# Optimization experiments

Hardware: AMD Instinct MI355X
Metric: run time of the kernel (lower is better)

The kernel has to match this reference:

```python
import jax, jax.numpy as jnp
import numpy as np
from jax import lax

L, D, H, F, T = 4, 512, 8, 2048, 1000
B, S = 8, 1024

def setup_inputs() -> dict:
    key = jax.random.key(0)
    ks = jax.random.split(key, 12)
    s = 0.02
    return {
        'features': jax.random.normal(ks[0], (B, S, D), jnp.float32),
        'Wq': jax.random.normal(ks[1], (L, D, D), jnp.float32) * s,
        'Wk': jax.random.normal(ks[2], (L, D, D), jnp.float32) * s,
        'Wv': jax.random.normal(ks[3], (L, D, D), jnp.float32) * s,
        'bq': jnp.zeros((L, D), jnp.float32),
        'bk': jnp.zeros((L, D), jnp.float32),
        'bv': jnp.zeros((L, D), jnp.float32),
        'Wo': jax.random.normal(ks[4], (L, D, D), jnp.float32) * s,
        'bo': jnp.zeros((L, D), jnp.float32),
        'ln1_g': jnp.ones((L, D), jnp.float32),
        'ln1_b': jnp.zeros((L, D), jnp.float32),
        'ln2_g': jnp.ones((L, D), jnp.float32),
        'ln2_b': jnp.zeros((L, D), jnp.float32),
        'W1': jax.random.normal(ks[5], (L, F, D), jnp.float32) * s,
        'b1': jnp.zeros((L, F), jnp.float32),
        'W2': jax.random.normal(ks[6], (L, D, F), jnp.float32) * s,
        'b2': jnp.zeros((L, D), jnp.float32),
        'Wout': jax.random.normal(ks[7], (D, D), jnp.float32) * s,
        'bout': jnp.zeros((D,), jnp.float32),
    }

def _layernorm(x, g, b, eps=1e-5):
    mu = jnp.mean(x, axis=-1, keepdims=True)
    var = jnp.var(x, axis=-1, keepdims=True)
    return (x - mu) / jnp.sqrt(var + eps) * g + b

def _ddim_noise(features):
    betas = jnp.linspace(1e-4, 0.02, T)
    alphas_cumprod = jnp.cumprod(1.0 - betas)
    base = jax.random.key(42)
    def step(x, t):
        a = alphas_cumprod[t]
        noise = jax.random.normal(jax.random.fold_in(base, t), x.shape, x.dtype)
        return jnp.sqrt(a) * x + jnp.sqrt(1.0 - a) * noise, None
    x, _ = lax.scan(step, features, jnp.arange(1, T))
    return x

def reference(features, Wq, Wk, Wv, bq, bk, bv, Wo, bo, ln1_g, ln1_b, ln2_g, ln2_b, W1, b1, W2, b2, Wout, bout):
    x = _ddim_noise(features)  # [B,S,D]
    dh = D // H
    scale = 1.0 / jnp.sqrt(jnp.float32(dh))
    for l in range(L):
        # multi-head self-attention (post-norm, no dropout at eval)
        q = (x @ Wq[l].T + bq[l]).reshape(B, S, H, dh).transpose(0, 2, 1, 3)
        k = (x @ Wk[l].T + bk[l]).reshape(B, S, H, dh).transpose(0, 2, 1, 3)
        v = (x @ Wv[l].T + bv[l]).reshape(B, S, H, dh).transpose(0, 2, 1, 3)
        scores = jnp.einsum('bhqd,bhkd->bhqk', q, k) * scale
        attn = jax.nn.softmax(scores, axis=-1)
        o = jnp.einsum('bhqk,bhkd->bhqd', attn, v).transpose(0, 2, 1, 3).reshape(B, S, D)
        o = o @ Wo[l].T + bo[l]
        x = _layernorm(x + o, ln1_g[l], ln1_b[l])
        # feed-forward (ReLU, PyTorch default)
        ff = jax.nn.relu(x @ W1[l].T + b1[l]) @ W2[l].T + b2[l]
        x = _layernorm(x + ff, ln2_g[l], ln2_b[l])
    return x @ Wout.T + bout
```

## Files before the change

### kernel.cpp

```cpp
#include <hip/hip_runtime.h>
#include <stdint.h>
#include <math.h>

typedef unsigned short u16;
typedef __bf16 bf16x8 __attribute__((ext_vector_type(8)));
typedef float f32x4 __attribute__((ext_vector_type(4)));
typedef short s16x8 __attribute__((ext_vector_type(8)));
union B8 { s16x8 s; bf16x8 b; };

__device__ __forceinline__ u16 f2bf(float f) {
    union { __bf16 h; u16 u; } r;
    r.h = (__bf16)f;
    return r.u;
}
__device__ __forceinline__ uint32_t pk2bf(float a, float b) {
    union { __bf16 h[2]; uint32_t u; } r;
    r.h[0] = (__bf16)a; r.h[1] = (__bf16)b;
    return r.u;
}
__device__ __forceinline__ float fexp2(float x) {
    return __builtin_amdgcn_exp2f(x);
}

typedef const __attribute__((address_space(1))) uint32_t* gas_t;
typedef __attribute__((address_space(3))) uint32_t* las_t;
__device__ __forceinline__ void gld16(const void* g, void* l) {
    __builtin_amdgcn_global_load_lds((gas_t)g, (las_t)l, 16, 0, 0);
}

__host__ __forceinline__ uint32_t rotl32(uint32_t x, int d) {
    return (x << d) | (x >> (32 - d));
}
__device__ __forceinline__ uint32_t rotl_d(uint32_t x, int d) {
    return __builtin_amdgcn_alignbit(x, x, (uint32_t)(32 - d));
}

__host__ inline void tf2x32_h(uint32_t k0, uint32_t k1, uint32_t& x0, uint32_t& x1) {
    uint32_t k2 = k0 ^ k1 ^ 0x1BD11BDAu;
    x0 += k0; x1 += k1;
    x0 += x1; x1 = rotl32(x1, 13); x1 ^= x0;
    x0 += x1; x1 = rotl32(x1, 15); x1 ^= x0;
    x0 += x1; x1 = rotl32(x1, 26); x1 ^= x0;
    x0 += x1; x1 = rotl32(x1,  6); x1 ^= x0;
    x0 += k1; x1 += k2 + 1u;
    x0 += x1; x1 = rotl32(x1, 17); x1 ^= x0;
    x0 += x1; x1 = rotl32(x1, 29); x1 ^= x0;
    x0 += x1; x1 = rotl32(x1, 16); x1 ^= x0;
    x0 += x1; x1 = rotl32(x1, 24); x1 ^= x0;
    x0 += k2; x1 += k0 + 2u;
    x0 += x1; x1 = rotl32(x1, 13); x1 ^= x0;
    x0 += x1; x1 = rotl32(x1, 15); x1 ^= x0;
    x0 += x1; x1 = rotl32(x1, 26); x1 ^= x0;
    x0 += x1; x1 = rotl32(x1,  6); x1 ^= x0;
    x0 += k0; x1 += k1 + 3u;
    x0 += x1; x1 = rotl32(x1, 17); x1 ^= x0;
    x0 += x1; x1 = rotl32(x1, 29); x1 ^= x0;
    x0 += x1; x1 = rotl32(x1, 16); x1 ^= x0;
    x0 += x1; x1 = rotl32(x1, 24); x1 ^= x0;
    x0 += k1; x1 += k2 + 4u;
    x0 += x1; x1 = rotl32(x1, 13); x1 ^= x0;
    x0 += x1; x1 = rotl32(x1, 15); x1 ^= x0;
    x0 += x1; x1 = rotl32(x1, 26); x1 ^= x0;
    x0 += x1; x1 = rotl32(x1,  6); x1 ^= x0;
    x0 += k2; x1 += k0 + 5u;
}

__device__ __forceinline__ void tf2x32_d(uint32_t k0, uint32_t k1,
                                         uint32_t& x0, uint32_t& x1) {
    uint32_t k2 = k0 ^ k1 ^ 0x1BD11BDAu;
    x0 += k0; x1 += k1;
    x0 += x1; x1 = rotl_d(x1, 13); x1 ^= x0;
    x0 += x1; x1 = rotl_d(x1, 15); x1 ^= x0;
    x0 += x1; x1 = rotl_d(x1, 26); x1 ^= x0;
    x0 += x1; x1 = rotl_d(x1,  6); x1 ^= x0;
    x0 += k1; x1 += k2 + 1u;
    x0 += x1; x1 = rotl_d(x1, 17); x1 ^= x0;
    x0 += x1; x1 = rotl_d(x1, 29); x1 ^= x0;
    x0 += x1; x1 = rotl_d(x1, 16); x1 ^= x0;
    x0 += x1; x1 = rotl_d(x1, 24); x1 ^= x0;
    x0 += k2; x1 += k0 + 2u;
    x0 += x1; x1 = rotl_d(x1, 13); x1 ^= x0;
    x0 += x1; x1 = rotl_d(x1, 15); x1 ^= x0;
    x0 += x1; x1 = rotl_d(x1, 26); x1 ^= x0;
    x0 += x1; x1 = rotl_d(x1,  6); x1 ^= x0;
    x0 += k0; x1 += k1 + 3u;
    x0 += x1; x1 = rotl_d(x1, 17); x1 ^= x0;
    x0 += x1; x1 = rotl_d(x1, 29); x1 ^= x0;
    x0 += x1; x1 = rotl_d(x1, 16); x1 ^= x0;
    x0 += x1; x1 = rotl_d(x1, 24); x1 ^= x0;
    x0 += k1; x1 += k2 + 4u;
    x0 += x1; x1 = rotl_d(x1, 13); x1 ^= x0;
    x0 += x1; x1 = rotl_d(x1, 15); x1 ^= x0;
    x0 += x1; x1 = rotl_d(x1, 26); x1 ^= x0;
    x0 += x1; x1 = rotl_d(x1,  6); x1 ^= x0;
    x0 += k2; x1 += k0 + 5u;
}

__device__ __forceinline__ float erfinv_f(float x) {
    float w = -__logf(fmaf(x, -x, 1.0f));
    float p;
    if (w < 5.0f) {
        w = w - 2.5f;
        p = 2.81022636e-08f;
        p = p * w + 3.43273939e-07f;
        p = p * w + -3.5233877e-06f;
        p = p * w + -4.39150654e-06f;
        p = p * w + 0.00021858087f;
        p = p * w + -0.00125372503f;
        p = p * w + -0.00417768164f;
        p = p * w + 0.246640727f;
        p = p * w + 1.50140941f;
    } else {
        w = sqrtf(w) - 3.0f;
        p = -0.000200214257f;
        p = p * w + 0.000100950558f;
        p = p * w + 0.00134934322f;
        p = p * w + -0.00367342844f;
        p = p * w + 0.00573950773f;
        p = p * w + -0.0076224613f;
        p = p * w + 0.00943887047f;
        p = p * w + 1.00167406f;
        p = p * w + 2.83297682f;
    }
    return p * x;
}

__device__ __forceinline__ float tf_normal(uint32_t k0, uint32_t k1, uint32_t idx) {
    uint32_t x0 = 0u, x1 = idx;
    tf2x32_d(k0, k1, x0, x1);
    uint32_t bits = x0 ^ x1;
    float f = __uint_as_float((bits >> 9) | 0x3f800000u) - 1.0f;
    float u = f * 2.0f - 0.99999994f;
    u = fmaxf(-0.99999994f, u);
    return 1.41421354f * erfinv_f(u);
}

__global__ __launch_bounds__(256) void noise_kernel(
    float* __restrict__ x, u16* __restrict__ xb,
    uint32_t ka0, uint32_t ka1, float ca,
    uint32_t kb0, uint32_t kb1, float cb, int n4)
{
    int i = blockIdx.x * 256 + threadIdx.x;
    if (i >= n4) return;
    float4 vx;
    ushort4 vb;
    #pragma unroll
    for (int e = 0; e < 4; ++e) {
        uint32_t idx = (uint32_t)(i * 4 + e);
        float a = ca * tf_normal(ka0, ka1, idx)
                + cb * tf_normal(kb0, kb1, idx);
        (&vx.x)[e] = a;
        (&vb.x)[e] = f2bf(a);
    }
    ((float4*)x)[i] = vx;
    ((ushort4*)xb)[i] = vb;
}

__global__ __launch_bounds__(256) void cvt_bf16_kernel(
    const float* __restrict__ s, u16* __restrict__ d, int n4)
{
    int i = blockIdx.x * 256 + threadIdx.x;
    if (i >= n4) return;
    float4 v = ((const float4*)s)[i];
    uint2 o;
    o.x = pk2bf(v.x, v.y);
    o.y = pk2bf(v.z, v.w);
    ((uint2*)d)[i] = o;
}

__global__ __launch_bounds__(256) void cvt_qkvw_kernel(
    const float* __restrict__ Wq, const float* __restrict__ Wk,
    const float* __restrict__ Wv, u16* __restrict__ dst, int n4)
{
    int i = blockIdx.x * 256 + threadIdx.x;
    if (i >= n4) return;
    int e = i * 4;
    int l = e / 786432;
    int rem = e - l * 786432;
    int sel = rem >> 18;
    int off = rem & 262143;
    const float* src = (sel == 0 ? Wq : sel == 1 ? Wk : Wv) + l * 262144 + off;
    float4 v = *(const float4*)src;
    uint2 o;
    o.x = pk2bf(v.x, v.y);
    o.y = pk2bf(v.z, v.w);
    *(uint2*)(dst + e) = o;
}

template<int TN, bool DBUF, bool QKV, bool RELU, bool RESID, bool BF16OUT>
__global__ __launch_bounds__(256) void gemm_bt(
    const u16* __restrict__ A, const u16* __restrict__ Bw,
    const float* __restrict__ bias0, const float* __restrict__ bias1,
    const float* __restrict__ bias2, const float* __restrict__ resid,
    void* __restrict__ out0, void* __restrict__ out1, void* __restrict__ out2,
    int M, int N, int K)
{
    constexpr int ACH = 16;
    constexpr int BCH = TN / 8;
    constexpr int CPW = (ACH + BCH) / 4;
    constexpr int NF = TN / 32;
    constexpr int NBUF = DBUF ? 2 : 1;
    constexpr int ASZ = 128 * 64;
    constexpr int BSZ = TN * 64;
    __shared__ __align__(16) u16 At[NBUF * ASZ];
    __shared__ __align__(16) u16 Bt[NBUF * BSZ];
    const int tid = threadIdx.x;
    const int l = tid & 63;
    const int w = tid >> 6;
    const int wr = w >> 1, wc = w & 1;

    int lid = blockIdx.y * gridDim.x + blockIdx.x;
    int nwg = gridDim.x * gridDim.y;
    int mb, nb;
    if ((nwg & 7) == 0) {
        int nlid = (lid & 7) * (nwg >> 3) + (lid >> 3);
        mb = nlid / gridDim.x;
        nb = nlid - mb * gridDim.x;
    } else { mb = blockIdx.y; nb = blockIdx.x; }

    const int lrow = l >> 3;
    const int lch  = (l & 7) ^ lrow;

    const u16* aTile = A  + (size_t)(mb * 128) * K + (size_t)lrow * K + lch * 8;
    const u16* bTile = Bw + (size_t)(nb * TN) * K + (size_t)lrow * K + lch * 8;

    f32x4 acc[4][NF] = {};

    auto stage = [&](int buf, int k0) {
        #pragma unroll
        for (int i = 0; i < CPW; ++i) {
            int c = w * CPW + i;
            if (c < ACH) gld16(aTile + (size_t)(c * 8) * K + k0, &At[buf * ASZ + c * 512]);
            else gld16(bTile + (size_t)((c - ACH) * 8) * K + k0, &Bt[buf * BSZ + (c - ACH) * 512]);
        }
    };
    auto compute = [&](int buf) {
        const u16* Ac = &At[buf * ASZ];
        const u16* Bc = &Bt[buf * BSZ];
        #pragma unroll
        for (int kc = 0; kc < 2; ++kc) {
            B8 af[4], bfr[NF];
            #pragma unroll
            for (int m = 0; m < 4; ++m) {
                int r = wr * 64 + m * 16 + (l & 15);
                int ch = kc * 4 + (l >> 4);
                af[m].s = *(const s16x8*)&Ac[r * 64 + ((ch ^ (r & 7)) * 8)];
            }
            #pragma unroll
            for (int n = 0; n < NF; ++n) {
                int r = wc * (TN / 2) + n * 16 + (l & 15);
                int ch = kc * 4 + (l >> 4);
                bfr[n].s = *(const s16x8*)&Bc[r * 64 + ((ch ^ (r & 7)) * 8)];
            }
            #pragma unroll
            for (int m = 0; m < 4; ++m)
                #pragma unroll
                for (int n = 0; n < NF; ++n)
                    acc[m][n] = __builtin_amdgcn_mfma_f32_16x16x32_bf16(
                        af[m].b, bfr[n].b, acc[m][n], 0, 0, 0);
        }
    };

    if constexpr (DBUF) {
        stage(0, 0);
        __syncthreads();
        int cur = 0;
        for (int k0 = 0; k0 < K; k0 += 64) {
            if (k0 + 64 < K) stage(cur ^ 1, k0 + 64);
            compute(cur);
            __syncthreads();
            cur ^= 1;
        }
    } else {
        for (int k0 = 0; k0 < K; k0 += 64) {
            stage(0, k0);
            __syncthreads();
            compute(0);
            __syncthreads();
        }
    }

    const float* biasp;
    void* outp;
    int colbase, Nout;
    float oscale = 1.0f;
    if constexpr (QKV) {
        int which = nb >> 2;
        colbase = (nb & 3) * 128 + wc * 64;
        if (which == 2) {
            float bcol[NF];
            #pragma unroll
            for (int n = 0; n < NF; ++n)
                bcol[n] = bias2[colbase + n * 16 + (l & 15)];
            u16* vT = (u16*)out2;
            #pragma unroll
            for (int m = 0; m < 4; ++m) {
                int row0 = mb * 128 + wr * 64 + m * 16 + (l >> 4) * 4;
                int bb = row0 >> 10, s0 = row0 & 1023;
                #pragma unroll
                for (int n = 0; n < NF; ++n) {
                    int col = colbase + n * 16 + (l & 15);
                    int hh = col >> 6, dd = col & 63;
                    uint2 o;
                    o.x = pk2bf(acc[m][n][0] + bcol[n], acc[m][n][1] + bcol[n]);
                    o.y = pk2bf(acc[m][n][2] + bcol[n], acc[m][n][3] + bcol[n]);
                    *(uint2*)&vT[((size_t)((bb * 8 + hh) * 64 + dd)) * 1024 + s0] = o;
                }
            }
            return;
        }
        biasp = which == 0 ? bias0 : bias1;
        outp  = which == 0 ? out0  : out1;
        if (which == 0) oscale = 0.18033688f;
        Nout = 512;
    } else {
        colbase = nb * TN + wc * (TN / 2);
        biasp = bias0;
        outp = out0;
        Nout = N;
    }

    float bcol[NF];
    #pragma unroll
    for (int n = 0; n < NF; ++n)
        bcol[n] = biasp[colbase + n * 16 + (l & 15)];

    #pragma unroll
    for (int m = 0; m < 4; ++m) {
        #pragma unroll
        for (int j = 0; j < 4; ++j) {
            int row = mb * 128 + wr * 64 + m * 16 + (l >> 4) * 4 + j;
            #pragma unroll
            for (int n = 0; n < NF; ++n) {
                int col = colbase + n * 16 + (l & 15);
                float v = acc[m][n][j] + bcol[n];
                if constexpr (QKV) v *= oscale;
                if constexpr (RESID) v += resid[(size_t)row * Nout + col];
                if constexpr (RELU)  v = fmaxf(v, 0.0f);
                if constexpr (BF16OUT) ((u16*)outp)[(size_t)row * Nout + col] = f2bf(v);
                else                   ((float*)outp)[(size_t)row * Nout + col] = v;
            }
        }
    }
}

template<bool RESID>
__global__ __launch_bounds__(512) void gemm64(
    const u16* __restrict__ A, const u16* __restrict__ Bw,
    const float* __restrict__ bias, const float* __restrict__ resid,
    float* __restrict__ out, int N, int K)
{
    constexpr int ACH = 16;
    constexpr int ASZ = 128 * 64, BSZ = 64 * 64;
    __shared__ __align__(16) u16 At[2 * ASZ];
    __shared__ __align__(16) u16 Bt[2 * BSZ];
    const int tid = threadIdx.x;
    const int l = tid & 63;
    const int w = tid >> 6;
    const int wr = w >> 1, wc = w & 1;

    int lid = blockIdx.y * gridDim.x + blockIdx.x;
    int nwg = gridDim.x * gridDim.y;
    int nlid = (lid & 7) * (nwg >> 3) + (lid >> 3);
    int mb = nlid / gridDim.x;
    int nb = nlid - mb * gridDim.x;

    const int lrow = l >> 3;
    const int lch  = (l & 7) ^ lrow;

    const u16* aTile = A  + (size_t)(mb * 128) * K + (size_t)lrow * K + lch * 8;
    const u16* bTile = Bw + (size_t)(nb * 64) * K + (size_t)lrow * K + lch * 8;

    f32x4 acc[2][2] = {};

    auto stage = [&](int buf, int k0) {
        #pragma unroll
        for (int i = 0; i < 3; ++i) {
            int c = w * 3 + i;
            if (c < ACH) gld16(aTile + (size_t)(c * 8) * K + k0, &At[buf * ASZ + c * 512]);
            else gld16(bTile + (size_t)((c - ACH) * 8) * K + k0, &Bt[buf * BSZ + (c - ACH) * 512]);
        }
    };
    auto compute = [&](int buf) {
        const u16* Ac = &At[buf * ASZ];
        const u16* Bc = &Bt[buf * BSZ];
        #pragma unroll
        for (int kc = 0; kc < 2; ++kc) {
            B8 af[2], bfr[2];
            #pragma unroll
            for (int m = 0; m < 2; ++m) {
                int r = wr * 32 + m * 16 + (l & 15);
                int ch = kc * 4 + (l >> 4);
                af[m].s = *(const s16x8*)&Ac[r * 64 + ((ch ^ (r & 7)) * 8)];
            }
            #pragma unroll
            for (int n = 0; n < 2; ++n) {
                int r = wc * 32 + n * 16 + (l & 15);
                int ch = kc * 4 + (l >> 4);
                bfr[n].s = *(const s16x8*)&Bc[r * 64 + ((ch ^ (r & 7)) * 8)];
            }
            #pragma unroll
            for (int m = 0; m < 2; ++m)
                #pragma unroll
                for (int n = 0; n < 2; ++n)
                    acc[m][n] = __builtin_amdgcn_mfma_f32_16x16x32_bf16(
                        af[m].b, bfr[n].b, acc[m][n], 0, 0, 0);
        }
    };

    stage(0, 0);
    __syncthreads();
    int cur = 0;
    for (int k0 = 0; k0 < K; k0 += 64) {
        if (k0 + 64 < K) stage(cur ^ 1, k0 + 64);
        compute(cur);
        __syncthreads();
        cur ^= 1;
    }

    float bcol[2];
    #pragma unroll
    for (int n = 0; n < 2; ++n)
        bcol[n] = bias[nb * 64 + wc * 32 + n * 16 + (l & 15)];

    #pragma unroll
    for (int m = 0; m < 2; ++m) {
        #pragma unroll
        for (int j = 0; j < 4; ++j) {
            int row = mb * 128 + wr * 32 + m * 16 + (l >> 4) * 4 + j;
            #pragma unroll
            for (int n = 0; n < 2; ++n) {
                int col = nb * 64 + wc * 32 + n * 16 + (l & 15);
                float v = acc[m][n][j] + bcol[n];
                if constexpr (RESID) v += resid[(size_t)row * N + col];
                out[(size_t)row * N + col] = v;
            }
        }
    }
}

__global__ __launch_bounds__(256) void ln_kernel(
    float* __restrict__ x, const float* __restrict__ g, const float* __restrict__ b,
    u16* __restrict__ xb)
{
    int row = blockIdx.x * 4 + (threadIdx.x >> 6);
    int l = threadIdx.x & 63;
    float4* xr = (float4*)(x + row * 512);
    float4 v0 = xr[l];
    float4 v1 = xr[l + 64];
    float s = v0.x + v0.y + v0.z + v0.w + v1.x + v1.y + v1.z + v1.w;
    float q = v0.x * v0.x + v0.y * v0.y + v0.z * v0.z + v0.w * v0.w
            + v1.x * v1.x + v1.y * v1.y + v1.z * v1.z + v1.w * v1.w;
    #pragma unroll
    for (int m = 1; m < 64; m <<= 1) {
        s += __shfl_xor(s, m, 64);
        q += __shfl_xor(q, m, 64);
    }
    float mean = s * (1.0f / 512.0f);
    float var  = q * (1.0f / 512.0f) - mean * mean;
    float rstd = rsqrtf(var + 1e-5f);
    const float4* gv = (const float4*)g;
    const float4* bv = (const float4*)b;
    float4 g0 = gv[l], g1 = gv[l + 64], b0 = bv[l], b1 = bv[l + 64];
    float4 o0, o1;
    o0.x = (v0.x - mean) * rstd * g0.x + b0.x;
    o0.y = (v0.y - mean) * rstd * g0.y + b0.y;
    o0.z = (v0.z - mean) * rstd * g0.z + b0.z;
    o0.w = (v0.w - mean) * rstd * g0.w + b0.w;
    o1.x = (v1.x - mean) * rstd * g1.x + b1.x;
    o1.y = (v1.y - mean) * rstd * g1.y + b1.y;
    o1.z = (v1.z - mean) * rstd * g1.z + b1.z;
    o1.w = (v1.w - mean) * rstd * g1.w + b1.w;
    xr[l] = o0; xr[l + 64] = o1;
    uint2 h0, h1;
    h0.x = pk2bf(o0.x, o0.y); h0.y = pk2bf(o0.z, o0.w);
    h1.x = pk2bf(o1.x, o1.y); h1.y = pk2bf(o1.z, o1.w);
    ((uint2*)(xb + row * 512))[l] = h0;
    ((uint2*)(xb + row * 512))[l + 64] = h1;
}

__global__ __launch_bounds__(512) void attn_kernel(
    const u16* __restrict__ Q, const u16* __restrict__ Km,
    const u16* __restrict__ vT, u16* __restrict__ O)
{
    __shared__ __align__(16) u16 Kt[2][64 * 64];
    __shared__ __align__(16) u16 Vt[2][64 * 64];
    __shared__ __align__(16) char Pl[8][4096];
    const int tid = threadIdx.x;
    const int l = tid & 63;
    const int w = tid >> 6;
    const int g = l >> 4;
    const int q15 = l & 15;
    const int bh = blockIdx.x;
    const int qb = blockIdx.y;
    const int b = bh >> 3, h = bh & 7;
    const int rowQ0 = b * 1024 + qb * 256 + w * 32;
    const int colh = h * 64;
    char* pl = &Pl[w][0];

    const int srow = l >> 3;
    const u16* Kbase = Km + (size_t)(b * 1024) * 512 + colh;
    const u16* Vbase = vT + (size_t)bh * 64 * 1024;

    B8 qf[2][2];
    #pragma unroll
    for (int qt = 0; qt < 2; ++qt)
        #pragma unroll
        for (int kc = 0; kc < 2; ++kc)
            qf[qt][kc].s = *(const s16x8*)&Q[(size_t)(rowQ0 + qt * 16 + q15) * 512
                                            + colh + kc * 32 + g * 8];

    f32x4 oacc[4][2] = {};
    float lrun[2] = {0.0f, 0.0f};

    auto stage = [&](int buf, int kt) {
        int r = w * 8 + srow;
        int cc = (l & 7) ^ (r & 7);
        gld16(Kbase + (size_t)(kt * 64 + r) * 512 + cc * 8, &Kt[buf][w * 512]);
        gld16(Vbase + (size_t)r * 1024 + kt * 64 + cc * 8, &Vt[buf][w * 512]);
    };

    stage(0, 0);
    __syncthreads();
    int cur = 0;

    for (int kt = 0; kt < 16; ++kt) {
        if (kt < 15) stage(cur ^ 1, kt + 1);
        const u16* KtL = &Kt[cur][0];
        const u16* VtL = &Vt[cur][0];

        f32x4 st[2][4];
        #pragma unroll
        for (int mt = 0; mt < 4; ++mt) {
            int r = mt * 16 + q15;
            B8 kf0, kf1;
            kf0.s = *(const s16x8*)&KtL[r * 64 + ((g ^ (r & 7)) * 8)];
            kf1.s = *(const s16x8*)&KtL[r * 64 + (((4 + g) ^ (r & 7)) * 8)];
            #pragma unroll
            for (int qt = 0; qt < 2; ++qt) {
                f32x4 t = {0.f, 0.f, 0.f, 0.f};
                t = __builtin_amdgcn_mfma_f32_16x16x32_bf16(kf0.b, qf[qt][0].b, t, 0, 0, 0);
                t = __builtin_amdgcn_mfma_f32_16x16x32_bf16(kf1.b, qf[qt][1].b, t, 0, 0, 0);
                st[qt][mt] = t;
            }
        }

        #pragma unroll
        for (int qt = 0; qt < 2; ++qt) {
            int qrow = qt * 16 + q15;
            int rbase = qrow * 128;
            int sw = (qrow & 7) << 4;
            float rs = 0.0f;
            #pragma unroll
            for (int mt = 0; mt < 4; ++mt) {
                float e0 = fexp2(st[qt][mt][0]);
                float e1 = fexp2(st[qt][mt][1]);
                float e2 = fexp2(st[qt][mt][2]);
                float e3 = fexp2(st[qt][mt][3]);
                rs += (e0 + e1) + (e2 + e3);
                uint2 pk;
                pk.x = pk2bf(e0, e1);
                pk.y = pk2bf(e2, e3);
                *(uint2*)(pl + rbase + ((mt * 32 + g * 8) ^ sw)) = pk;
            }
            rs += __shfl_xor(rs, 16, 64);
            rs += __shfl_xor(rs, 32, 64);
            lrun[qt] += rs;
        }

        B8 pf[2][2];
        #pragma unroll
        for (int qt = 0; qt < 2; ++qt) {
            int qrow = qt * 16 + q15;
            int sw = (qrow & 7) << 4;
            pf[qt][0].s = *(const s16x8*)(pl + qrow * 128 + ((g * 16) ^ sw));
            pf[qt][1].s = *(const s16x8*)(pl + qrow * 128 + (((4 + g) * 16) ^ sw));
        }

        #pragma unroll
        for (int dt = 0; dt < 4; ++dt) {
            int r = dt * 16 + q15;
            B8 vf0, vf1;
            vf0.s = *(const s16x8*)&VtL[r * 64 + ((g ^ (r & 7)) * 8)];
            vf1.s = *(const s16x8*)&VtL[r * 64 + (((4 + g) ^ (r & 7)) * 8)];
            #pragma unroll
            for (int qt = 0; qt < 2; ++qt) {
                oacc[dt][qt] = __builtin_amdgcn_mfma_f32_16x16x32_bf16(
                    vf0.b, pf[qt][0].b, oacc[dt][qt], 0, 0, 0);
                oacc[dt][qt] = __builtin_amdgcn_mfma_f32_16x16x32_bf16(
                    vf1.b, pf[qt][1].b, oacc[dt][qt], 0, 0, 0);
            }
        }
        __syncthreads();
        cur ^= 1;
    }

    #pragma unroll
    for (int qt = 0; qt < 2; ++qt) {
        float inv = 1.0f / lrun[qt];
        int row = rowQ0 + qt * 16 + q15;
        #pragma unroll
        for (int dt = 0; dt < 4; ++dt) {
            uint2 o;
            o.x = pk2bf(oacc[dt][qt][0] * inv, oacc[dt][qt][1] * inv);
            o.y = pk2bf(oacc[dt][qt][2] * inv, oacc[dt][qt][3] * inv);
            *(uint2*)&O[(size_t)row * 512 + colh + dt * 16 + g * 4] = o;
        }
    }
}

extern "C" void kernel_launch(void* const* d_in, const int* in_sizes, int n_in,
                              void* d_out, int out_size, void* d_ws, size_t ws_size,
                              hipStream_t stream)
{
    const int D = 512, F = 2048, Lc = 4;
    const int Mrows = 8 * 1024;

    const float* Wq   = (const float*)d_in[1];
    const float* Wk   = (const float*)d_in[2];
    const float* Wv   = (const float*)d_in[3];
    const float* bq   = (const float*)d_in[4];
    const float* bk   = (const float*)d_in[5];
    const float* bv   = (const float*)d_in[6];
    const float* Wo   = (const float*)d_in[7];
    const float* bo   = (const float*)d_in[8];
    const float* ln1g = (const float*)d_in[9];
    const float* ln1b = (const float*)d_in[10];
    const float* ln2g = (const float*)d_in[11];
    const float* ln2b = (const float*)d_in[12];
    const float* W1   = (const float*)d_in[13];
    const float* b1   = (const float*)d_in[14];
    const float* W2   = (const float*)d_in[15];
    const float* b2   = (const float*)d_in[16];
    const float* Wout = (const float*)d_in[17];
    const float* bout = (const float*)d_in[18];

    char* p = (char*)d_ws;
    auto alloc = [&](size_t bytes) {
        char* r = p;
        p += (bytes + 255) & ~(size_t)255;
        return r;
    };
    float* xA = (float*)alloc((size_t)Mrows * D * 4);
    float* xB = (float*)alloc((size_t)Mrows * D * 4);
    u16* xb   = (u16*)alloc((size_t)Mrows * D * 2);
    char* pool = alloc((size_t)Mrows * F * 2);
    u16* qb_ = (u16*)pool;
    u16* kb_ = (u16*)(pool + (size_t)Mrows * D * 2);
    u16* vT  = (u16*)(pool + (size_t)Mrows * D * 2 * 2);
    u16* ao  = (u16*)(pool + (size_t)Mrows * D * 2 * 3);
    u16* ff1 = (u16*)pool;
    u16* wqkvB = (u16*)alloc((size_t)Lc * 3 * D * D * 2);
    u16* woB   = (u16*)alloc((size_t)Lc * D * D * 2);
    u16* w1B   = (u16*)alloc((size_t)Lc * F * D * 2);
    u16* w2B   = (u16*)alloc((size_t)Lc * D * F * 2);
    u16* woutB = (u16*)alloc((size_t)D * D * 2);

    auto cvt = [&](const float* src, u16* dst, size_t n) {
        int n4 = (int)(n / 4);
        cvt_bf16_kernel<<<(n4 + 255) / 256, 256, 0, stream>>>(src, dst, n4);
    };
    {
        int n4 = Lc * 3 * D * D / 4;
        cvt_qkvw_kernel<<<(n4 + 255) / 256, 256, 0, stream>>>(Wq, Wk, Wv, wqkvB, n4);
    }
    cvt(Wo, woB, (size_t)Lc * D * D);
    cvt(W1, w1B, (size_t)Lc * F * D);
    cvt(W2, w2B, (size_t)Lc * D * F);
    cvt(Wout, woutB, (size_t)D * D);

    float ac[1000];
    {
        float start = 1e-4f, stop = 0.02f;
        float delta = (stop - start) / 999.0f;
        float prod = 1.0f;
        for (int i = 0; i < 1000; ++i) {
            float beta = start + (float)i * delta;
            prod *= (1.0f - beta);
            ac[i] = prod;
        }
    }
    int ts[2] = {999, 998};
    double cs[2];
    double tail = 1.0;
    for (int idx = 0; idx < 2; ++idx) {
        int t = ts[idx];
        cs[idx] = sqrt(1.0 - (double)ac[t]) * tail;
        tail *= sqrt((double)ac[t]);
    }
    uint32_t kk[2][2];
    for (int idx = 0; idx < 2; ++idx) {
        uint32_t x0 = 0u, x1 = (uint32_t)ts[idx];
        tf2x32_h(0u, 42u, x0, x1);
        kk[idx][0] = x0; kk[idx][1] = x1;
    }
    int n4tot = Mrows * D / 4;
    noise_kernel<<<(n4tot + 255) / 256, 256, 0, stream>>>(
        xA, xb,
        kk[0][0], kk[0][1], (float)cs[0],
        kk[1][0], kk[1][1], (float)cs[1], n4tot);

    dim3 gqkv(3 * D / 128, Mrows / 128);
    dim3 g64(D / 64, Mrows / 128);
    dim3 gff1(F / 128, Mrows / 128);

    for (int l = 0; l < Lc; ++l) {
        const u16* wqkv_l = wqkvB + (size_t)l * 3 * D * D;
        const u16* wo_l = woB + (size_t)l * D * D;
        const u16* w1_l = w1B + (size_t)l * F * D;
        const u16* w2_l = w2B + (size_t)l * D * F;

        gemm_bt<128, false, true, false, false, true><<<gqkv, 256, 0, stream>>>(
            xb, wqkv_l, bq + l * D, bk + l * D, bv + l * D, nullptr,
            qb_, kb_, vT, Mrows, 3 * D, D);
        attn_kernel<<<dim3(64, 4), 512, 0, stream>>>(qb_, kb_, vT, ao);
        gemm64<true><<<g64, 512, 0, stream>>>(
            ao, wo_l, bo + l * D, xA, xB, D, D);
        ln_kernel<<<Mrows / 4, 256, 0, stream>>>(xB, ln1g + l * D, ln1b + l * D, xb);
        gemm_bt<128, false, false, true, false, true><<<gff1, 256, 0, stream>>>(
            xb, w1_l, b1 + l * F, nullptr, nullptr, nullptr,
            ff1, nullptr, nullptr, Mrows, F, D);
        gemm64<true><<<g64, 512, 0, stream>>>(
            ff1, w2_l, b2 + l * D, xB, xA, D, F);
        ln_kernel<<<Mrows / 4, 256, 0, stream>>>(xA, ln2g + l * D, ln2b + l * D, xb);
    }
    gemm64<false><<<g64, 512, 0, stream>>>(
        xb, woutB, bout, nullptr, (float*)d_out, D, D);
}
```

Baseline: 616.1 us.

## Keep residual stream in bf16 and fuse weight conversions into one kernel

Drops the fp32 copies of the hidden state and uses the existing bf16 buffer as the residual input. The output projections now write bf16 pre-norm sums, and layernorm reads bf16 and writes only bf16. The five weight-conversion launches become a single kernel over one contiguous buffer. This cuts global memory traffic and launch count, but keeping the residual in bf16 loses precision across layers. Unused double-buffer template paths are also removed.

```diff
diff --git a/kernel.cpp b/kernel.cpp
--- a/kernel.cpp
+++ b/kernel.cpp
@@ -17,6 +17,9 @@
     union { __bf16 h[2]; uint32_t u; } r;
     r.h[0] = (__bf16)a; r.h[1] = (__bf16)b;
     return r.u;
+}
+__device__ __forceinline__ float bf2f(u16 u) {
+    return __uint_as_float(((uint32_t)u) << 16);
 }
 __device__ __forceinline__ float fexp2(float x) {
     return __builtin_amdgcn_exp2f(x);
@@ -136,50 +139,43 @@
 }
 
 __global__ __launch_bounds__(256) void noise_kernel(
-    float* __restrict__ x, u16* __restrict__ xb,
+    u16* __restrict__ xb,
     uint32_t ka0, uint32_t ka1, float ca,
     uint32_t kb0, uint32_t kb1, float cb, int n4)
 {
     int i = blockIdx.x * 256 + threadIdx.x;
     if (i >= n4) return;
-    float4 vx;
     ushort4 vb;
     #pragma unroll
     for (int e = 0; e < 4; ++e) {
         uint32_t idx = (uint32_t)(i * 4 + e);
         float a = ca * tf_normal(ka0, ka1, idx)
                 + cb * tf_normal(kb0, kb1, idx);
-        (&vx.x)[e] = a;
         (&vb.x)[e] = f2bf(a);
     }
-    ((float4*)x)[i] = vx;
     ((ushort4*)xb)[i] = vb;
 }
 
-__global__ __launch_bounds__(256) void cvt_bf16_kernel(
-    const float* __restrict__ s, u16* __restrict__ d, int n4)
-{
-    int i = blockIdx.x * 256 + threadIdx.x;
-    if (i >= n4) return;
-    float4 v = ((const float4*)s)[i];
-    uint2 o;
-    o.x = pk2bf(v.x, v.y);
-    o.y = pk2bf(v.z, v.w);
-    ((uint2*)d)[i] = o;
-}
-
-__global__ __launch_bounds__(256) void cvt_qkvw_kernel(
+__global__ __launch_bounds__(256) void cvt_all_kernel(
     const float* __restrict__ Wq, const float* __restrict__ Wk,
-    const float* __restrict__ Wv, u16* __restrict__ dst, int n4)
+    const float* __restrict__ Wv, const float* __restrict__ Wo,
+    const float* __restrict__ W1, const float* __restrict__ W2,
+    const float* __restrict__ Wout, u16* __restrict__ dst, int n4)
 {
     int i = blockIdx.x * 256 + threadIdx.x;
     if (i >= n4) return;
     int e = i * 4;
-    int l = e / 786432;
-    int rem = e - l * 786432;
-    int sel = rem >> 18;
-    int off = rem & 262143;
-    const float* src = (sel == 0 ? Wq : sel == 1 ? Wk : Wv) + l * 262144 + off;
+    const float* src;
+    if (e < 3145728) {
+        int l = e / 786432;
+        int rem = e - l * 786432;
+        int sel = rem >> 18;
+        int off = rem & 262143;
+        src = (sel == 0 ? Wq : sel == 1 ? Wk : Wv) + l * 262144 + off;
+    } else if (e < 4194304) src = Wo + (e - 3145728);
+    else if (e < 8388608)  src = W1 + (e - 4194304);
+    else if (e < 12582912) src = W2 + (e - 8388608);
+    else                   src = Wout + (e - 12582912);
     float4 v = *(const float4*)src;
     uint2 o;
     o.x = pk2bf(v.x, v.y);
@@ -187,11 +183,11 @@
     *(uint2*)(dst + e) = o;
 }
 
-template<int TN, bool DBUF, bool QKV, bool RELU, bool RESID, bool BF16OUT>
+template<int TN, bool QKV, bool RELU>
 __global__ __launch_bounds__(256) void gemm_bt(
     const u16* __restrict__ A, const u16* __restrict__ Bw,
     const float* __restrict__ bias0, const float* __restrict__ bias1,
-    const float* __restrict__ bias2, const float* __restrict__ resid,
+    const float* __restrict__ bias2,
     void* __restrict__ out0, void* __restrict__ out1, void* __restrict__ out2,
     int M, int N, int K)
 {
@@ -199,11 +195,10 @@
     constexpr int BCH = TN / 8;
     constexpr int CPW = (ACH + BCH) / 4;
     constexpr int NF = TN / 32;
-    constexpr int NBUF = DBUF ? 2 : 1;
     constexpr int ASZ = 128 * 64;
     constexpr int BSZ = TN * 64;
-    __shared__ __align__(16) u16 At[NBUF * ASZ];
-    __shared__ __align__(16) u16 Bt[NBUF * BSZ];
+    __shared__ __align__(16) u16 At[ASZ];
+    __shared__ __align__(16) u16 Bt[BSZ];
     const int tid = threadIdx.x;
     const int l = tid & 63;
     const int w = tid >> 6;
@@ -226,17 +221,14 @@
 
     f32x4 acc[4][NF] = {};
 
-    auto stage = [&](int buf, int k0) {
+    for (int k0 = 0; k0 < K; k0 += 64) {
         #pragma unroll
         for (int i = 0; i < CPW; ++i) {
             int c = w * CPW + i;
-            if (c < ACH) gld16(aTile + (size_t)(c * 8) * K + k0, &At[buf * ASZ + c * 512]);
-            else gld16(bTile + (size_t)((c - ACH) * 8) * K + k0, &Bt[buf * BSZ + (c - ACH) * 512]);
-        }
-    };
-    auto compute = [&](int buf) {
-        const u16* Ac = &At[buf * ASZ];
-        const u16* Bc = &Bt[buf * BSZ];
+            if (c < ACH) gld16(aTile + (size_t)(c * 8) * K + k0, &At[c * 512]);
+            else gld16(bTile + (size_t)((c - ACH) * 8) * K + k0, &Bt[(c - ACH) * 512]);
+        }
+        __syncthreads();
         #pragma unroll
         for (int kc = 0; kc < 2; ++kc) {
             B8 af[4], bfr[NF];
@@ -244,13 +236,13 @@
             for (int m = 0; m < 4; ++m) {
                 int r = wr * 64 + m * 16 + (l & 15);
                 int ch = kc * 4 + (l >> 4);
-                af[m].s = *(const s16x8*)&Ac[r * 64 + ((ch ^ (r & 7)) * 8)];
+                af[m].s = *(const s16x8*)&At[r * 64 + ((ch ^ (r & 7)) * 8)];
             }
             #pragma unroll
             for (int n = 0; n < NF; ++n) {
                 int r = wc * (TN / 2) + n * 16 + (l & 15);
                 int ch = kc * 4 + (l >> 4);
-                bfr[n].s = *(const s16x8*)&Bc[r * 64 + ((ch ^ (r & 7)) * 8)];
+                bfr[n].s = *(const s16x8*)&Bt[r * 64 + ((ch ^ (r & 7)) * 8)];
             }
             #pragma unroll
             for (int m = 0; m < 4; ++m)
@@ -259,25 +251,7 @@
                     acc[m][n] = __builtin_amdgcn_mfma_f32_16x16x32_bf16(
                         af[m].b, bfr[n].b, acc[m][n], 0, 0, 0);
         }
-    };
-
-    if constexpr (DBUF) {
-        stage(0, 0);
         __syncthreads();
-        int cur = 0;
-        for (int k0 = 0; k0 < K; k0 += 64) {
-            if (k0 + 64 < K) stage(cur ^ 1, k0 + 64);
-            compute(cur);
-            __syncthreads();
-            cur ^= 1;
-        }
-    } else {
-        for (int k0 = 0; k0 < K; k0 += 64) {
-            stage(0, k0);
-            __syncthreads();
-            compute(0);
-            __syncthreads();
-        }
     }
 
     const float* biasp;
@@ -335,20 +309,18 @@
                 int col = colbase + n * 16 + (l & 15);
                 float v = acc[m][n][j] + bcol[n];
                 if constexpr (QKV) v *= oscale;
-                if constexpr (RESID) v += resid[(size_t)row * Nout + col];
                 if constexpr (RELU)  v = fmaxf(v, 0.0f);
-                if constexpr (BF16OUT) ((u16*)outp)[(size_t)row * Nout + col] = f2bf(v);
-                else                   ((float*)outp)[(size_t)row * Nout + col] = v;
-            }
-        }
-    }
-}
-
-template<bool RESID>
+                ((u16*)outp)[(size_t)row * Nout + col] = f2bf(v);
+            }
+        }
+    }
+}
+
+template<bool RESID, bool BF16OUT>
 __global__ __launch_bounds__(512) void gemm64(
     const u16* __restrict__ A, const u16* __restrict__ Bw,
-    const float* __restrict__ bias, const float* __restrict__ resid,
-    float* __restrict__ out, int N, int K)
+    const float* __restrict__ bias, const u16* __restrict__ resid,
+    void* __restrict__ out, int N, int K)
 {
     constexpr int ACH = 16;
     constexpr int ASZ = 128 * 64, BSZ = 64 * 64;
@@ -432,25 +404,31 @@
             for (int n = 0; n < 2; ++n) {
                 int col = nb * 64 + wc * 32 + n * 16 + (l & 15);
                 float v = acc[m][n][j] + bcol[n];
-                if constexpr (RESID) v += resid[(size_t)row * N + col];
-                out[(size_t)row * N + col] = v;
+                if constexpr (RESID) v += bf2f(resid[(size_t)row * N + col]);
+                if constexpr (BF16OUT) ((u16*)out)[(size_t)row * N + col] = f2bf(v);
+                else                   ((float*)out)[(size_t)row * N + col] = v;
             }
         }
     }
 }
 
 __global__ __launch_bounds__(256) void ln_kernel(
-    float* __restrict__ x, const float* __restrict__ g, const float* __restrict__ b,
-    u16* __restrict__ xb)
+    const u16* __restrict__ y, const float* __restrict__ g,
+    const float* __restrict__ b, u16* __restrict__ xb)
 {
     int row = blockIdx.x * 4 + (threadIdx.x >> 6);
     int l = threadIdx.x & 63;
-    float4* xr = (float4*)(x + row * 512);
-    float4 v0 = xr[l];
-    float4 v1 = xr[l + 64];
-    float s = v0.x + v0.y + v0.z + v0.w + v1.x + v1.y + v1.z + v1.w;
-    float q = v0.x * v0.x + v0.y * v0.y + v0.z * v0.z + v0.w * v0.w
-            + v1.x * v1.x + v1.y * v1.y + v1.z * v1.z + v1.w * v1.w;
+    uint4 vv = ((const uint4*)(y + (size_t)row * 512))[l];
+    uint32_t wsr[4] = {vv.x, vv.y, vv.z, vv.w};
+    float xv[8];
+    #pragma unroll
+    for (int k = 0; k < 4; ++k) {
+        xv[2 * k]     = __uint_as_float(wsr[k] << 16);
+        xv[2 * k + 1] = __uint_as_float(wsr[k] & 0xFFFF0000u);
+    }
+    float s = 0.0f, q = 0.0f;
+    #pragma unroll
+    for (int k = 0; k < 8; ++k) { s += xv[k]; q += xv[k] * xv[k]; }
     #pragma unroll
     for (int m = 1; m < 64; m <<= 1) {
         s += __shfl_xor(s, m, 64);
@@ -461,22 +439,23 @@
     float rstd = rsqrtf(var + 1e-5f);
     const float4* gv = (const float4*)g;
     const float4* bv = (const float4*)b;
-    float4 g0 = gv[l], g1 = gv[l + 64], b0 = bv[l], b1 = bv[l + 64];
-    float4 o0, o1;
-    o0.x = (v0.x - mean) * rstd * g0.x + b0.x;
-    o0.y = (v0.y - mean) * rstd * g0.y + b0.y;
-    o0.z = (v0.z - mean) * rstd * g0.z + b0.z;
-    o0.w = (v0.w - mean) * rstd * g0.w + b0.w;
-    o1.x = (v1.x - mean) * rstd * g1.x + b1.x;
-    o1.y = (v1.y - mean) * rstd * g1.y + b1.y;
-    o1.z = (v1.z - mean) * rstd * g1.z + b1.z;
-    o1.w = (v1.w - mean) * rstd * g1.w + b1.w;
-    xr[l] = o0; xr[l + 64] = o1;
-    uint2 h0, h1;
-    h0.x = pk2bf(o0.x, o0.y); h0.y = pk2bf(o0.z, o0.w);
-    h1.x = pk2bf(o1.x, o1.y); h1.y = pk2bf(o1.z, o1.w);
-    ((uint2*)(xb + row * 512))[l] = h0;
-    ((uint2*)(xb + row * 512))[l + 64] = h1;
+    float4 g0 = gv[2 * l], g1 = gv[2 * l + 1];
+    float4 b0 = bv[2 * l], b1 = bv[2 * l + 1];
+    float ov[8];
+    ov[0] = (xv[0] - mean) * rstd * g0.x + b0.x;
+    ov[1] = (xv[1] - mean) * rstd * g0.y + b0.y;
+    ov[2] = (xv[2] - mean) * rstd * g0.z + b0.z;
+    ov[3] = (xv[3] - mean) * rstd * g0.w + b0.w;
+    ov[4] = (xv[4] - mean) * rstd * g1.x + b1.x;
+    ov[5] = (xv[5] - mean) * rstd * g1.y + b1.y;
+    ov[6] = (xv[6] - mean) * rstd * g1.z + b1.z;
+    ov[7] = (xv[7] - mean) * rstd * g1.w + b1.w;
+    uint4 o;
+    o.x = pk2bf(ov[0], ov[1]);
+    o.y = pk2bf(ov[2], ov[3]);
+    o.z = pk2bf(ov[4], ov[5]);
+    o.w = pk2bf(ov[6], ov[7]);
+    ((uint4*)(xb + (size_t)row * 512))[l] = o;
 }
 
 __global__ __launch_bounds__(512) void attn_kernel(
@@ -641,33 +620,26 @@
         p += (bytes + 255) & ~(size_t)255;
         return r;
     };
-    float* xA = (float*)alloc((size_t)Mrows * D * 4);
-    float* xB = (float*)alloc((size_t)Mrows * D * 4);
-    u16* xb   = (u16*)alloc((size_t)Mrows * D * 2);
+    u16* xb = (u16*)alloc((size_t)Mrows * D * 2);
+    u16* y  = (u16*)alloc((size_t)Mrows * D * 2);
     char* pool = alloc((size_t)Mrows * F * 2);
     u16* qb_ = (u16*)pool;
     u16* kb_ = (u16*)(pool + (size_t)Mrows * D * 2);
     u16* vT  = (u16*)(pool + (size_t)Mrows * D * 2 * 2);
     u16* ao  = (u16*)(pool + (size_t)Mrows * D * 2 * 3);
     u16* ff1 = (u16*)pool;
-    u16* wqkvB = (u16*)alloc((size_t)Lc * 3 * D * D * 2);
-    u16* woB   = (u16*)alloc((size_t)Lc * D * D * 2);
-    u16* w1B   = (u16*)alloc((size_t)Lc * F * D * 2);
-    u16* w2B   = (u16*)alloc((size_t)Lc * D * F * 2);
-    u16* woutB = (u16*)alloc((size_t)D * D * 2);
-
-    auto cvt = [&](const float* src, u16* dst, size_t n) {
-        int n4 = (int)(n / 4);
-        cvt_bf16_kernel<<<(n4 + 255) / 256, 256, 0, stream>>>(src, dst, n4);
-    };
+    u16* wAll  = (u16*)alloc((size_t)12845056 * 2);
+    u16* wqkvB = wAll;
+    u16* woB   = wAll + 3145728;
+    u16* w1B   = wAll + 4194304;
+    u16* w2B   = wAll + 8388608;
+    u16* woutB = wAll + 12582912;
+
     {
-        int n4 = Lc * 3 * D * D / 4;
-        cvt_qkvw_kernel<<<(n4 + 255) / 256, 256, 0, stream>>>(Wq, Wk, Wv, wqkvB, n4);
-    }
-    cvt(Wo, woB, (size_t)Lc * D * D);
-    cvt(W1, w1B, (size_t)Lc * F * D);
-    cvt(W2, w2B, (size_t)Lc * D * F);
-    cvt(Wout, woutB, (size_t)D * D);
+        int n4 = 12845056 / 4;
+        cvt_all_kernel<<<(n4 + 255) / 256, 256, 0, stream>>>(
+            Wq, Wk, Wv, Wo, W1, W2, Wout, wAll, n4);
+    }
 
     float ac[1000];
     {
@@ -696,7 +668,7 @@
     }
     int n4tot = Mrows * D / 4;
     noise_kernel<<<(n4tot + 255) / 256, 256, 0, stream>>>(
-        xA, xb,
+        xb,
         kk[0][0], kk[0][1], (float)cs[0],
         kk[1][0], kk[1][1], (float)cs[1], n4tot);
 
@@ -710,20 +682,20 @@
         const u16* w1_l = w1B + (size_t)l * F * D;
         const u16* w2_l = w2B + (size_t)l * D * F;
 
-        gemm_bt<128, false, true, false, false, true><<<gqkv, 256, 0, stream>>>(
-            xb, wqkv_l, bq + l * D, bk + l * D, bv + l * D, nullptr,
+        gemm_bt<128, true, false><<<gqkv, 256, 0, stream>>>(
+            xb, wqkv_l, bq + l * D, bk + l * D, bv + l * D,
             qb_, kb_, vT, Mrows, 3 * D, D);
         attn_kernel<<<dim3(64, 4), 512, 0, stream>>>(qb_, kb_, vT, ao);
-        gemm64<true><<<g64, 512, 0, stream>>>(
-            ao, wo_l, bo + l * D, xA, xB, D, D);
-        ln_kernel<<<Mrows / 4, 256, 0, stream>>>(xB, ln1g + l * D, ln1b + l * D, xb);
-        gemm_bt<128, false, false, true, false, true><<<gff1, 256, 0, stream>>>(
-            xb, w1_l, b1 + l * F, nullptr, nullptr, nullptr,
+        gemm64<true, true><<<g64, 512, 0, stream>>>(
+            ao, wo_l, bo + l * D, xb, y, D, D);
+        ln_kernel<<<Mrows / 4, 256, 0, stream>>>(y, ln1g + l * D, ln1b + l * D, xb);
+        gemm_bt<128, false, true><<<gff1, 256, 0, stream>>>(
+            xb, w1_l, b1 + l * F, nullptr, nullptr,
             ff1, nullptr, nullptr, Mrows, F, D);
-        gemm64<true><<<g64, 512, 0, stream>>>(
-            ff1, w2_l, b2 + l * D, xB, xA, D, F);
-        ln_kernel<<<Mrows / 4, 256, 0, stream>>>(xA, ln2g + l * D, ln2b + l * D, xb);
-    }
-    gemm64<false><<<g64, 512, 0, stream>>>(
+        gemm64<true, true><<<g64, 512, 0, stream>>>(
+            ff1, w2_l, b2 + l * D, xb, y, D, F);
+        ln_kernel<<<Mrows / 4, 256, 0, stream>>>(y, ln2g + l * D, ln2b + l * D, xb);
+    }
+    gemm64<false, false><<<g64, 512, 0, stream>>>(
         xb, woutB, bout, nullptr, (float*)d_out, D, D);
 }
```

Result: no change. 607.2 us (-1.4%).
